# Optimization experiments

Measured on AMD Instinct MI355X. Metric: run time of the kernel, lower is better.

## Reference

```python
import jax, jax.numpy as jnp
import numpy as np
import math

B, N, DIM, H, DH = 4, 1024, 512, 8, 64
INNER = H * DH
TEMP = 0.1
REG_LAMBDA = 0.3
LARGE_NEG = -1.0e9


def setup_inputs() -> dict:
    key = jax.random.key(0)
    ks = jax.random.split(key, 10)
    x = jax.random.normal(ks[0], (B, N, DIM), dtype=jnp.float32)
    # binary channel mask with guaranteed self-connection on the diagonal
    m = jax.random.randint(ks[1], (B, N, N), 0, 2, dtype=jnp.int32)
    eye_i = jnp.eye(N, dtype=jnp.int32)[None]
    attn_mask = jnp.maximum(m, eye_i)
    s = 0.02
    Wq = jax.random.normal(ks[2], (DIM, INNER), dtype=jnp.float32) * s
    bq = jnp.zeros((INNER,), dtype=jnp.float32)
    Wk = jax.random.normal(ks[3], (DIM, INNER), dtype=jnp.float32) * s
    bk = jnp.zeros((INNER,), dtype=jnp.float32)
    Wv = jax.random.normal(ks[4], (DIM, INNER), dtype=jnp.float32) * s
    bv = jnp.zeros((INNER,), dtype=jnp.float32)
    Wo = jax.random.normal(ks[5], (INNER, DIM), dtype=jnpp_dummy()) * s if False else jax.random.normal(ks[5], (INNER, DIM), dtype=jnp.float32) * s
    bo = jnp.zeros((DIM,), dtype=jnp.float32)
    return {"x": x, "attn_mask": attn_mask, "Wq": Wq, "bq": bq, "Wk": Wk,
            "bk": bk, "Wv": Wv, "bv": bv, "Wo": Wo, "bo": bo}


def jnp_dummy():
    return jnp.float32


def _split_heads(t):
    # [b, n, h*d] -> [b, h, n, d]
    return t.reshape(t.shape[0], t.shape[1], H, DH).transpose(0, 2, 1, 3)


def _dynamical_contrastive_loss(scores, attn_mask_f, norm_matrix):
    # cosine similarity matrix (scores / |q||k|)
    cos = scores / norm_matrix
    e = jnp.exp(cos / TEMP)                                   # [b,h,n,n]
    pos = (e * attn_mask_f[:, None]).sum(-1)                  # [b,h,n]
    allsum = e.sum(-1)                                        # [b,h,n]
    clustering = -jnp.log(pos / allsum)
    eye = jnp.eye(N, dtype=attn_mask_f.dtype)
    regular = jnp.abs(attn_mask_f - eye[None]).sum((-2, -1)) / (N * (N - 1))
    return clustering.mean() + REG_LAMBDA * regular.mean()


def reference(x, attn_mask, Wq, bq, Wk, bk, Wv, bv, Wo, bo):
    q = _split_heads(x @ Wq + bq)  # [b,h,n,d]
    k = _split_heads(x @ Wk + bk)
    v = _split_heads(x @ Wv + bv)
    scale = 1.0 / math.sqrt(DH)

    scores = jnp.einsum('bhid,bhjd->bhij', q, k)
    q_norm = jnp.linalg.norm(q, axis=-1, keepdims=True)       # [b,h,n,1]
    k_norm = jnp.linalg.norm(k, axis=-1, keepdims=True)
    norm_matrix = q_norm * jnp.swapaxes(k_norm, -1, -2)       # [b,h,n,n]

    am = attn_mask.astype(scores.dtype)[:, None]              # [b,1,n,n]
    masked_scores = scores * am + (1.0 - am) * LARGE_NEG
    # faithful replication of the all-blocked-row special case
    # (-1e9 is finite so this is a no-op unless scores contain -inf)
    row_all_blocked = jnp.all(jnp.isneginf(masked_scores), axis=-1, keepdims=True)
    masked_scores = jnp.where(row_all_blocked, jnp.zeros_like(masked_scores), masked_scores)

    dcl = _dynamical_contrastive_loss(scores, attn_mask.astype(scores.dtype), norm_matrix)

    attn = jax.nn.softmax(masked_scores * scale, axis=-1)
    out = jnp.einsum('bhij,bhjd->bhid', attn, v)
    out = out.transpose(0, 2, 1, 3).reshape(x.shape[0], x.shape[1], INNER)
    # dropout is identity in eval mode
    return out @ Wo + bo, attn, dcl
```

## Files before the change

### kernel.cpp

```cpp
#include <hip/hip_runtime.h>
#include <hip/hip_bf16.h>
#include <math.h>

#define BB 4
#define NTOK 1024
#define DIMD 512
#define HH 8
#define DH 64
#define INNER 512
#define BH (BB*HH)
#define ROWS (BB*NTOK)
#define SCALE 0.125f
#define INV_TEMP 10.0f

typedef __bf16 bf16_t;
using bf16x4 = __attribute__((ext_vector_type(4))) __bf16;
using bf16x8 = __attribute__((ext_vector_type(8))) __bf16;
using f32x4  = __attribute__((ext_vector_type(4))) float;

__device__ __forceinline__ int swz(int row, int e) { return e ^ ((row & 7) << 3); }

__device__ __forceinline__ void gload_lds16(const bf16_t* g, bf16_t* l)
{
    __builtin_amdgcn_global_load_lds(
        (const __attribute__((address_space(1))) void*)g,
        (__attribute__((address_space(3))) void*)l, 16, 0, 0);
}

template<int TM, int TN, int MT, int NT>
__device__ __forceinline__ void gemm_core(
    const bf16_t* __restrict__ A, int ldA,
    const bf16_t* __restrict__ B, int ldB, int K,
    bf16_t* As, bf16_t* Bs, f32x4 (&acc)[MT][NT])
{
    const int t = threadIdx.x;
    const int w = t >> 6, l = t & 63;
    constexpr int WGN = TN / (NT * 16);
    const int wm = w / WGN, wn = w % WGN;
    const int lrow = l & 15, lk = (l >> 4) * 8;
    constexpr int ASZ = TM * 32, BSZ = TN * 32;

    auto stage = [&](int k0, int buf) {
        #pragma unroll
        for (int it = 0; it < TM / 64; ++it)
            gload_lds16(&A[(size_t)((t >> 2) + it * 64) * ldA + k0 + (t & 3) * 8],
                        As + buf * ASZ + ((size_t)it * 256 + w * 64) * 8);
        #pragma unroll
        for (int it = 0; it < TN / 64; ++it)
            gload_lds16(&B[(size_t)((t >> 2) + it * 64) * ldB + k0 + (t & 3) * 8],
                        Bs + buf * BSZ + ((size_t)it * 256 + w * 64) * 8);
    };

    stage(0, 0);
    __syncthreads();
    for (int k0 = 0; k0 < K; k0 += 32) {
        const int cur = (k0 >> 5) & 1;
        if (k0 + 32 < K) stage(k0 + 32, cur ^ 1);
        const bf16_t* Ac = As + cur * ASZ;
        const bf16_t* Bc = Bs + cur * BSZ;
        bf16x8 af[MT], bf[NT];
        #pragma unroll
        for (int mt = 0; mt < MT; ++mt)
            af[mt] = *(const bf16x8*)&Ac[(wm * MT * 16 + mt * 16 + lrow) * 32 + lk];
        #pragma unroll
        for (int nt = 0; nt < NT; ++nt)
            bf[nt] = *(const bf16x8*)&Bc[(wn * NT * 16 + nt * 16 + lrow) * 32 + lk];
        #pragma unroll
        for (int mt = 0; mt < MT; ++mt)
            #pragma unroll
            for (int nt = 0; nt < NT; ++nt)
                acc[mt][nt] = __builtin_amdgcn_mfma_f32_16x16x32_bf16(
                    af[mt], bf[nt], acc[mt][nt], 0, 0, 0);
        __syncthreads();
    }
}

__global__ __launch_bounds__(256) void prep_kernel(
    const float* __restrict__ x,
    const float* __restrict__ Wq, const float* __restrict__ Wk,
    const float* __restrict__ Wv, const float* __restrict__ Wo,
    const int* __restrict__ mask,
    bf16_t* __restrict__ xb, bf16_t* __restrict__ wt,
    unsigned int* __restrict__ mp)
{
    __shared__ float tile[32][33];
    const int bid = blockIdx.x, t = threadIdx.x;
    if (bid < 2048) {
        int idx = bid * 256 + t;
        float4 v = ((const float4*)x)[idx];
        bf16x4 o = { (bf16_t)v.x, (bf16_t)v.y, (bf16_t)v.z, (bf16_t)v.w };
        ((bf16x4*)xb)[idx] = o;
    } else if (bid < 3072) {
        int f = bid - 2048;
        int bx = f & 15, by = (f >> 4) & 15, z = f >> 8;
        const float* src = (z == 0) ? Wq : (z == 1) ? Wk : (z == 2) ? Wv : Wo;
        bf16_t* dst = wt + (size_t)z * DIMD * INNER;
        const int tx = t & 31, ty = t >> 5;
        const int rBase = by * 32, cBase = bx * 32;
        #pragma unroll
        for (int i = 0; i < 4; ++i)
            tile[ty + i * 8][tx] = src[(size_t)(rBase + ty + i * 8) * INNER + cBase + tx];
        __syncthreads();
        #pragma unroll
        for (int i = 0; i < 4; ++i)
            dst[(size_t)(cBase + ty + i * 8) * DIMD + rBase + tx] = (bf16_t)tile[tx][ty + i * 8];
    } else {
        int f = bid - 3072;
        int rr = f & 255, b = f >> 8;
        const int* mb = mask + ((size_t)(b * NTOK + rr * 4)) * NTOK;
        #pragma unroll
        for (int u = 0; u < 4; ++u) {
            int col = u * 256 + t;
            unsigned int o = (unsigned)mb[col]
                           | ((unsigned)mb[NTOK + col] << 8)
                           | ((unsigned)mb[2 * NTOK + col] << 16)
                           | ((unsigned)mb[3 * NTOK + col] << 24);
            mp[((size_t)b * 256 + rr) * NTOK + col] = o;
        }
    }
}

__global__ __launch_bounds__(256) void qkv_gemm(
    const bf16_t* __restrict__ xb, const bf16_t* __restrict__ wt,
    const float* __restrict__ bq, const float* __restrict__ bk,
    const float* __restrict__ bv,
    bf16_t* __restrict__ qb, bf16_t* __restrict__ kb, bf16_t* __restrict__ vt,
    float* __restrict__ iqn, float* __restrict__ ikn)
{
    __shared__ __align__(16) bf16_t As[2 * 64 * 32];
    __shared__ __align__(16) bf16_t Bs[2 * 128 * 32];
    const int z = blockIdx.z;
    const bf16_t* Bp = wt + (size_t)z * DIMD * INNER;
    const float* bias = (z == 0) ? bq : (z == 1) ? bk : bv;
    const int rowBase = blockIdx.y * 64, colBase = blockIdx.x * 128;

    f32x4 acc[2][4] = {};
    gemm_core<64, 128, 2, 4>(xb + (size_t)rowBase * DIMD, DIMD,
                             Bp + (size_t)colBase * DIMD, DIMD, DIMD,
                             As, Bs, acc);

    const int l = threadIdx.x & 63, w = threadIdx.x >> 6;
    const int wm = w >> 1, wn = w & 1;
    float nsum[2][4] = {};
    #pragma unroll
    for (int mt = 0; mt < 2; ++mt)
        #pragma unroll
        for (int nt = 0; nt < 4; ++nt)
            #pragma unroll
            for (int r = 0; r < 4; ++r) {
                int grow = rowBase + wm * 32 + mt * 16 + (l >> 4) * 4 + r;
                int gcol = colBase + wn * 64 + nt * 16 + (l & 15);
                float val = acc[mt][nt][r] + bias[gcol];
                bf16_t vb16 = (bf16_t)val;
                int b = grow >> 10, n = grow & 1023, h = gcol >> 6, d = gcol & 63;
                if (z == 0)
                    qb[(((size_t)b * HH + h) * NTOK + n) * DH + d] = vb16;
                else if (z == 1)
                    kb[(((size_t)b * HH + h) * NTOK + n) * DH + d] = vb16;
                else
                    vt[(((size_t)b * HH + h) * DH + d) * NTOK + n] = vb16;
                if (z < 2) { float vb = (float)vb16; nsum[mt][r] += vb * vb; }
            }
    if (z < 2) {
        float* dst = (z == 0) ? iqn : ikn;
        const int h = (colBase >> 6) + wn;
        #pragma unroll
        for (int mt = 0; mt < 2; ++mt)
            #pragma unroll
            for (int r = 0; r < 4; ++r) {
                float s = nsum[mt][r];
                s += __shfl_xor(s, 8); s += __shfl_xor(s, 4);
                s += __shfl_xor(s, 2); s += __shfl_xor(s, 1);
                if ((l & 15) == 0) {
                    int grow = rowBase + wm * 32 + mt * 16 + (l >> 4) * 4 + r;
                    int b = grow >> 10, n = grow & 1023;
                    dst[((size_t)b * HH + h) * NTOK + n] = 1.0f / sqrtf(s);
                }
            }
    }
}

__global__ __launch_bounds__(512) void attn_fused(
    const bf16_t* __restrict__ qb, const bf16_t* __restrict__ kb,
    const bf16_t* __restrict__ vt, const unsigned int* __restrict__ mp,
    const float* __restrict__ iqn, const float* __restrict__ ikn,
    float* __restrict__ attnf, bf16_t* __restrict__ ctxb,
    float* __restrict__ cl, float* __restrict__ rg)
{
    __shared__ __align__(16) bf16_t KV[2][2][64 * 64];
    __shared__ __align__(16) bf16_t Ps[8][16 * 64];
    __shared__ float4 sred[8][16];
    const int bh = blockIdx.y;
    const int b = bh >> 3, h = bh & 7;
    const int rowBase = blockIdx.x * 64;
    const bf16_t* Q = qb + (size_t)bh * NTOK * DH;
    const bf16_t* K = kb + (size_t)bh * NTOK * DH;
    const bf16_t* V = vt + (size_t)bh * DH * NTOK;
    const float* iknr = ikn + (size_t)bh * NTOK;
    const int t = threadIdx.x, w = t >> 6, l = t & 63;
    const int half = w >> 2, rw = w & 3;
    const int l15 = l & 15, q = l >> 4;
    bf16_t* Pw = Ps[w];

    auto stageK = [&](int tt, int buf) {
        #pragma unroll
        for (int u = 0; u < 2; ++u) {
            int g = (u * 8 + w) * 64 + l;
            int hh = g >> 9, kr = (g >> 3) & 63, ci = g & 7;
            gload_lds16(K + (size_t)(hh * 512 + tt * 64 + kr) * DH + ((ci * 8) ^ ((kr & 7) << 3)),
                        &KV[buf][0][0] + (size_t)(u * 8 + w) * 512);
        }
    };
    auto stageV = [&](int tt, int buf) {
        #pragma unroll
        for (int u = 0; u < 2; ++u) {
            int g = (u * 8 + w) * 64 + l;
            int hh = g >> 9, d = (g >> 3) & 63, ci = g & 7;
            gload_lds16(V + (size_t)d * NTOK + hh * 512 + tt * 64 + ((ci * 8) ^ ((d & 7) << 3)),
                        &KV[buf][0][0] + (size_t)(u * 8 + w) * 512);
        }
    };

    bf16x8 af[2];
    {
        const bf16_t* qrow = Q + (size_t)(rowBase + rw * 16 + l15) * DH + q * 8;
        af[0] = *(const bf16x8*)(qrow);
        af[1] = *(const bf16x8*)(qrow + 32);
    }
    const int tok = rowBase + rw * 16 + q * 4;
    float iqn4[4];
    #pragma unroll
    for (int r = 0; r < 4; ++r)
        iqn4[r] = iqn[(size_t)bh * NTOK + tok + r];
    const unsigned int* mrow = mp + ((size_t)b * 256 + (tok >> 2)) * NTOK;

    f32x4 sacc[8][4] = {};
    unsigned int mmc[8][4];
    float alls[4] = {}, pos[4] = {}, esum[4] = {}, regf[4] = {};

    stageK(0, 0);
    __syncthreads();
    #pragma unroll
    for (int tt = 0; tt < 8; ++tt) {
        const int col0 = half * 512 + tt * 64;
        if (tt < 7) stageK(tt + 1, (tt + 1) & 1);
        float ik4[4];
        #pragma unroll
        for (int nt = 0; nt < 4; ++nt) {
            int c = col0 + nt * 16 + l15;
            mmc[tt][nt] = mrow[c];
            ik4[nt] = iknr[c];
        }
        const bf16_t* Kh = &KV[tt & 1][half][0];
        #pragma unroll
        for (int ks = 0; ks < 2; ++ks) {
            int koff = ks * 32 + q * 8;
            #pragma unroll
            for (int nt = 0; nt < 4; ++nt) {
                int kr = nt * 16 + l15;
                bf16x8 bfk = *(const bf16x8*)&Kh[kr * 64 + swz(kr, koff)];
                sacc[tt][nt] = __builtin_amdgcn_mfma_f32_16x16x32_bf16(af[ks], bfk, sacc[tt][nt], 0, 0, 0);
            }
        }
        #pragma unroll
        for (int nt = 0; nt < 4; ++nt) {
            float ik = ik4[nt];
            unsigned int mm = mmc[tt][nt];
            #pragma unroll
            for (int r = 0; r < 4; ++r) {
                float s = sacc[tt][nt][r];
                float mbit = (float)((mm >> (8 * r)) & 1u);
                float e1 = __expf(s * iqn4[r] * ik * INV_TEMP);
                float e2 = __expf(s * SCALE);
                alls[r] += e1;
                pos[r]  += e1 * mbit;
                esum[r] += e2 * mbit;
                regf[r] += mbit;
            }
        }
        __syncthreads();
    }
    #pragma unroll
    for (int r = 0; r < 4; ++r) {
        #pragma unroll
        for (int off = 8; off; off >>= 1) {
            alls[r] += __shfl_xor(alls[r], off);
            pos[r]  += __shfl_xor(pos[r], off);
            esum[r] += __shfl_xor(esum[r], off);
            regf[r] += __shfl_xor(regf[r], off);
        }
    }
    if (l15 == 0) {
        #pragma unroll
        for (int r = 0; r < 4; ++r)
            sred[w][q * 4 + r] = make_float4(alls[r], pos[r], esum[r], regf[r]);
    }
    __syncthreads();
    float inv4[4];
    #pragma unroll
    for (int r = 0; r < 4; ++r) {
        float4 o = sred[w ^ 4][q * 4 + r];
        float allsT = alls[r] + o.x;
        float posT  = pos[r]  + o.y;
        float esumT = esum[r] + o.z;
        float regT  = regf[r] + o.w;
        inv4[r] = 1.0f / esumT;
        if (half == 0 && l15 == 0) {
            int rowG = bh * NTOK + tok + r;
            cl[rowG] = logf(allsT) - logf(posT);
            if (h == 0) rg[b * NTOK + tok + r] = regT - 1.0f;
        }
    }

    float* prow = attnf + ((size_t)bh * NTOK + tok) * NTOK;
    f32x4 cacc[4] = {};
    stageV(0, 0);
    __syncthreads();
    #pragma unroll
    for (int tt = 0; tt < 8; ++tt) {
        const int col0 = half * 512 + tt * 64;
        if (tt < 7) stageV(tt + 1, (tt + 1) & 1);
        #pragma unroll
        for (int nt = 0; nt < 4; ++nt) {
            int c = nt * 16 + l15;
            unsigned int mm = mmc[tt][nt];
            #pragma unroll
            for (int r = 0; r < 4; ++r) {
                float p = ((mm >> (8 * r)) & 1u)
                        ? __expf(sacc[tt][nt][r] * SCALE) * inv4[r] : 0.0f;
                prow[(size_t)r * NTOK + col0 + c] = p;
                int pr = q * 4 + r;
                Pw[pr * 64 + swz(pr, c)] = (bf16_t)p;
            }
        }
        const bf16_t* Vh = &KV[tt & 1][half][0];
        #pragma unroll
        for (int ks = 0; ks < 2; ++ks) {
            int koff = ks * 32 + q * 8;
            bf16x8 afp = *(const bf16x8*)&Pw[l15 * 64 + swz(l15, koff)];
            #pragma unroll
            for (int nt = 0; nt < 4; ++nt) {
                int d = nt * 16 + l15;
                bf16x8 bfv = *(const bf16x8*)&Vh[d * 64 + swz(d, koff)];
                cacc[nt] = __builtin_amdgcn_mfma_f32_16x16x32_bf16(afp, bfv, cacc[nt], 0, 0, 0);
            }
        }
        __syncthreads();
    }
    float* cred = (float*)&Ps[0][0];
    if (half == 1) {
        #pragma unroll
        for (int nt = 0; nt < 4; ++nt)
            #pragma unroll
            for (int r = 0; r < 4; ++r)
                cred[(size_t)rw * 1024 + (q * 4 + r) * 64 + nt * 16 + l15] = cacc[nt][r];
    }
    __syncthreads();
    if (half == 0) {
        #pragma unroll
        for (int nt = 0; nt < 4; ++nt)
            #pragma unroll
            for (int r = 0; r < 4; ++r) {
                float v = cacc[nt][r] + cred[(size_t)rw * 1024 + (q * 4 + r) * 64 + nt * 16 + l15];
                int n = tok + r;
                int d = nt * 16 + l15;
                ctxb[((size_t)b * NTOK + n) * INNER + h * DH + d] = (bf16_t)v;
            }
    }
}

__device__ __forceinline__ float block_sum(float v, float* sh)
{
    #pragma unroll
    for (int off = 32; off; off >>= 1) v += __shfl_down(v, off);
    __syncthreads();
    if ((threadIdx.x & 63) == 0) sh[threadIdx.x >> 6] = v;
    __syncthreads();
    return sh[0] + sh[1] + sh[2] + sh[3];
}

__global__ __launch_bounds__(256) void out_gemm(
    const bf16_t* __restrict__ ctxb, const bf16_t* __restrict__ wt,
    const float* __restrict__ bo, float* __restrict__ outp,
    const float* __restrict__ cl, const float* __restrict__ rg,
    float* __restrict__ dcl)
{
    __shared__ __align__(16) bf16_t As[2 * 64 * 32];
    __shared__ __align__(16) bf16_t Bs[2 * 128 * 32];
    __shared__ float sh4[4];
    const int rowBase = blockIdx.y * 64, colBase = blockIdx.x * 128;
    const bf16_t* Wot = wt + (size_t)3 * DIMD * INNER;

    f32x4 acc[2][4] = {};
    gemm_core<64, 128, 2, 4>(ctxb + (size_t)rowBase * INNER, INNER,
                             Wot + (size_t)colBase * INNER, INNER, INNER,
                             As, Bs, acc);

    const int l = threadIdx.x & 63, w = threadIdx.x >> 6;
    const int wm = w >> 1, wn = w & 1;
    #pragma unroll
    for (int mt = 0; mt < 2; ++mt)
        #pragma unroll
        for (int nt = 0; nt < 4; ++nt)
            #pragma unroll
            for (int r = 0; r < 4; ++r) {
                int grow = rowBase + wm * 32 + mt * 16 + (l >> 4) * 4 + r;
                int gcol = colBase + wn * 64 + nt * 16 + (l & 15);
                outp[(size_t)grow * DIMD + gcol] = acc[mt][nt][r] + bo[gcol];
            }

    if (blockIdx.x == 0 && blockIdx.y == 0) {
        float s1 = 0.f, s2 = 0.f;
        for (int idx = threadIdx.x; idx < BH * NTOK; idx += 256) s1 += cl[idx];
        for (int idx = threadIdx.x; idx < BB * NTOK; idx += 256) s2 += rg[idx];
        __syncthreads();
        s1 = block_sum(s1, sh4);
        s2 = block_sum(s2, sh4);
        if (threadIdx.x == 0) {
            dcl[0] = s1 * (1.0f / (float)(BB * HH * NTOK))
                   + 0.3f * s2 * (1.0f / ((float)NTOK * (float)(NTOK - 1) * (float)BB));
        }
    }
}

extern "C" void kernel_launch(void* const* d_in, const int* in_sizes, int n_in,
                              void* d_out, int out_size, void* d_ws, size_t ws_size,
                              hipStream_t stream)
{
    const float* x  = (const float*)d_in[0];
    const int* mask = (const int*)d_in[1];
    const float* Wq = (const float*)d_in[2];
    const float* bq = (const float*)d_in[3];
    const float* Wk = (const float*)d_in[4];
    const float* bk = (const float*)d_in[5];
    const float* Wv = (const float*)d_in[6];
    const float* bv = (const float*)d_in[7];
    const float* Wo = (const float*)d_in[8];
    const float* bo = (const float*)d_in[9];

    float* out   = (float*)d_out;
    float* attnf = out + (size_t)ROWS * DIMD;
    float* dcl   = attnf + (size_t)BH * NTOK * NTOK;

    char* wsb = (char*)d_ws;
    bf16_t* xb    = (bf16_t*)wsb;
    bf16_t* wt    = xb + (size_t)ROWS * DIMD;
    bf16_t* qb    = wt + (size_t)4 * DIMD * INNER;
    bf16_t* kb    = qb + (size_t)BH * NTOK * DH;
    bf16_t* vt    = kb + (size_t)BH * NTOK * DH;
    bf16_t* ctxb  = vt + (size_t)BH * NTOK * DH;
    float*  iqn   = (float*)(ctxb + (size_t)ROWS * INNER);
    float*  ikn   = iqn + BH * NTOK;
    float*  cl    = ikn + BH * NTOK;
    float*  rg    = cl + BH * NTOK;
    unsigned int* mpk = (unsigned int*)(rg + BB * NTOK);

    dim3 blk(256);
    prep_kernel<<<dim3(4096), blk, 0, stream>>>(x, Wq, Wk, Wv, Wo, mask, xb, wt, mpk);
    qkv_gemm<<<dim3(4, 64, 3), blk, 0, stream>>>(xb, wt, bq, bk, bv, qb, kb, vt, iqn, ikn);
    attn_fused<<<dim3(16, 32), dim3(512), 0, stream>>>(qb, kb, vt, mpk, iqn, ikn, attnf, ctxb, cl, rg);
    out_gemm<<<dim3(4, 64), blk, 0, stream>>>(ctxb, wt, bo, out, cl, rg, dcl);
}
```

Baseline: 282.7 us.

## Recompute QK scores in second pass instead of holding them in registers

Drops the 128-float score array and cached mask words that were kept in registers between the statistics pass and the probability/PV pass. The second pass now reloads K tiles and the mask and recomputes the QK MFMAs, which lowers register pressure and may allow higher occupancy. It also removes double buffering and full unrolling, so each tile's global-to-LDS load is followed by a barrier with no overlap. The cost is doubled QK compute and K traffic, plus exposed load latency.

```diff
diff --git a/kernel.cpp b/kernel.cpp
--- a/kernel.cpp
+++ b/kernel.cpp
@@ -187,7 +187,8 @@
     float* __restrict__ attnf, bf16_t* __restrict__ ctxb,
     float* __restrict__ cl, float* __restrict__ rg)
 {
-    __shared__ __align__(16) bf16_t KV[2][2][64 * 64];
+    __shared__ __align__(16) bf16_t Ks[2][64 * 64];
+    __shared__ __align__(16) bf16_t Vs[2][64 * 64];
     __shared__ __align__(16) bf16_t Ps[8][16 * 64];
     __shared__ float4 sred[8][16];
     const int bh = blockIdx.y;
@@ -202,25 +203,6 @@
     const int l15 = l & 15, q = l >> 4;
     bf16_t* Pw = Ps[w];
 
-    auto stageK = [&](int tt, int buf) {
-        #pragma unroll
-        for (int u = 0; u < 2; ++u) {
-            int g = (u * 8 + w) * 64 + l;
-            int hh = g >> 9, kr = (g >> 3) & 63, ci = g & 7;
-            gload_lds16(K + (size_t)(hh * 512 + tt * 64 + kr) * DH + ((ci * 8) ^ ((kr & 7) << 3)),
-                        &KV[buf][0][0] + (size_t)(u * 8 + w) * 512);
-        }
-    };
-    auto stageV = [&](int tt, int buf) {
-        #pragma unroll
-        for (int u = 0; u < 2; ++u) {
-            int g = (u * 8 + w) * 64 + l;
-            int hh = g >> 9, d = (g >> 3) & 63, ci = g & 7;
-            gload_lds16(V + (size_t)d * NTOK + hh * 512 + tt * 64 + ((ci * 8) ^ ((d & 7) << 3)),
-                        &KV[buf][0][0] + (size_t)(u * 8 + w) * 512);
-        }
-    };
-
     bf16x8 af[2];
     {
         const bf16_t* qrow = Q + (size_t)(rowBase + rw * 16 + l15) * DH + q * 8;
@@ -234,41 +216,43 @@
         iqn4[r] = iqn[(size_t)bh * NTOK + tok + r];
     const unsigned int* mrow = mp + ((size_t)b * 256 + (tok >> 2)) * NTOK;
 
-    f32x4 sacc[8][4] = {};
-    unsigned int mmc[8][4];
     float alls[4] = {}, pos[4] = {}, esum[4] = {}, regf[4] = {};
 
-    stageK(0, 0);
-    __syncthreads();
-    #pragma unroll
     for (int tt = 0; tt < 8; ++tt) {
         const int col0 = half * 512 + tt * 64;
-        if (tt < 7) stageK(tt + 1, (tt + 1) & 1);
-        float ik4[4];
+        #pragma unroll
+        for (int u = 0; u < 2; ++u) {
+            int g = (u * 8 + w) * 64 + l;
+            int hh = g >> 9, kr = (g >> 3) & 63, ci = g & 7;
+            gload_lds16(K + (size_t)(hh * 512 + tt * 64 + kr) * DH + ((ci * 8) ^ ((kr & 7) << 3)),
+                        &Ks[0][0] + (size_t)(u * 8 + w) * 512);
+        }
+        unsigned int mm4[4]; float ik4[4];
         #pragma unroll
         for (int nt = 0; nt < 4; ++nt) {
             int c = col0 + nt * 16 + l15;
-            mmc[tt][nt] = mrow[c];
+            mm4[nt] = mrow[c];
             ik4[nt] = iknr[c];
         }
-        const bf16_t* Kh = &KV[tt & 1][half][0];
+        __syncthreads();
+        f32x4 sacc[4] = {};
         #pragma unroll
         for (int ks = 0; ks < 2; ++ks) {
             int koff = ks * 32 + q * 8;
             #pragma unroll
             for (int nt = 0; nt < 4; ++nt) {
                 int kr = nt * 16 + l15;
-                bf16x8 bfk = *(const bf16x8*)&Kh[kr * 64 + swz(kr, koff)];
-                sacc[tt][nt] = __builtin_amdgcn_mfma_f32_16x16x32_bf16(af[ks], bfk, sacc[tt][nt], 0, 0, 0);
+                bf16x8 bfk = *(const bf16x8*)&Ks[half][kr * 64 + swz(kr, koff)];
+                sacc[nt] = __builtin_amdgcn_mfma_f32_16x16x32_bf16(af[ks], bfk, sacc[nt], 0, 0, 0);
             }
         }
         #pragma unroll
         for (int nt = 0; nt < 4; ++nt) {
             float ik = ik4[nt];
-            unsigned int mm = mmc[tt][nt];
-            #pragma unroll
-            for (int r = 0; r < 4; ++r) {
-                float s = sacc[tt][nt][r];
+            unsigned int mm = mm4[nt];
+            #pragma unroll
+            for (int r = 0; r < 4; ++r) {
+                float s = sacc[nt][r];
                 float mbit = (float)((mm >> (8 * r)) & 1u);
                 float e1 = __expf(s * iqn4[r] * ik * INV_TEMP);
                 float e2 = __expf(s * SCALE);
@@ -314,26 +298,51 @@
 
     float* prow = attnf + ((size_t)bh * NTOK + tok) * NTOK;
     f32x4 cacc[4] = {};
-    stageV(0, 0);
-    __syncthreads();
-    #pragma unroll
     for (int tt = 0; tt < 8; ++tt) {
         const int col0 = half * 512 + tt * 64;
-        if (tt < 7) stageV(tt + 1, (tt + 1) & 1);
+        #pragma unroll
+        for (int u = 0; u < 2; ++u) {
+            int g = (u * 8 + w) * 64 + l;
+            int hh = g >> 9, kr = (g >> 3) & 63, ci = g & 7;
+            gload_lds16(K + (size_t)(hh * 512 + tt * 64 + kr) * DH + ((ci * 8) ^ ((kr & 7) << 3)),
+                        &Ks[0][0] + (size_t)(u * 8 + w) * 512);
+        }
+        #pragma unroll
+        for (int u = 0; u < 2; ++u) {
+            int g = (u * 8 + w) * 64 + l;
+            int hh = g >> 9, d = (g >> 3) & 63, ci = g & 7;
+            gload_lds16(V + (size_t)d * NTOK + hh * 512 + tt * 64 + ((ci * 8) ^ ((d & 7) << 3)),
+                        &Vs[0][0] + (size_t)(u * 8 + w) * 512);
+        }
+        unsigned int mm4[4];
+        #pragma unroll
+        for (int nt = 0; nt < 4; ++nt)
+            mm4[nt] = mrow[col0 + nt * 16 + l15];
+        __syncthreads();
+        f32x4 sacc[4] = {};
+        #pragma unroll
+        for (int ks = 0; ks < 2; ++ks) {
+            int koff = ks * 32 + q * 8;
+            #pragma unroll
+            for (int nt = 0; nt < 4; ++nt) {
+                int kr = nt * 16 + l15;
+                bf16x8 bfk = *(const bf16x8*)&Ks[half][kr * 64 + swz(kr, koff)];
+                sacc[nt] = __builtin_amdgcn_mfma_f32_16x16x32_bf16(af[ks], bfk, sacc[nt], 0, 0, 0);
+            }
+        }
         #pragma unroll
         for (int nt = 0; nt < 4; ++nt) {
             int c = nt * 16 + l15;
-            unsigned int mm = mmc[tt][nt];
+            unsigned int mm = mm4[nt];
             #pragma unroll
             for (int r = 0; r < 4; ++r) {
                 float p = ((mm >> (8 * r)) & 1u)
-                        ? __expf(sacc[tt][nt][r] * SCALE) * inv4[r] : 0.0f;
+                        ? __expf(sacc[nt][r] * SCALE) * inv4[r] : 0.0f;
                 prow[(size_t)r * NTOK + col0 + c] = p;
                 int pr = q * 4 + r;
                 Pw[pr * 64 + swz(pr, c)] = (bf16_t)p;
             }
         }
-        const bf16_t* Vh = &KV[tt & 1][half][0];
         #pragma unroll
         for (int ks = 0; ks < 2; ++ks) {
             int koff = ks * 32 + q * 8;
@@ -341,7 +350,7 @@
             #pragma unroll
             for (int nt = 0; nt < 4; ++nt) {
                 int d = nt * 16 + l15;
-                bf16x8 bfv = *(const bf16x8*)&Vh[d * 64 + swz(d, koff)];
+                bf16x8 bfv = *(const bf16x8*)&Vs[half][d * 64 + swz(d, koff)];
                 cacc[nt] = __builtin_amdgcn_mfma_f32_16x16x32_bf16(afp, bfv, cacc[nt], 0, 0, 0);
             }
         }
```

Result: faster. 271.1 us (-4.1%).
